# Performance work log

Measured on AMD Instinct MI355X. Metric: run time of the kernel, lower is better.

## Reference

```python
import jax, jax.numpy as jnp
import numpy as np

B, T, D = 16, 2048, 512
NUM_CODES = 8192
BETA = 0.25


def setup_inputs() -> dict:
    key = jax.random.key(0)
    k1, k2 = jax.random.split(key)
    z_e = jax.random.normal(k1, (B, T, D), dtype=jnp.float32)
    # nn.init.uniform_(weight, -1/num_codes, 1/num_codes)
    lim = 1.0 / NUM_CODES
    codebook = jax.random.uniform(k2, (NUM_CODES, D), dtype=jnp.float32,
                                  minval=-lim, maxval=lim)
    return {"z_e": z_e, "codebook": codebook}


def reference(z_e, codebook):
    b, t, d = z_e.shape
    flat = z_e.reshape(b * t, d)                      # [BT, D]
    dist = (jnp.sum(flat * flat, axis=1, keepdims=True)
            - 2.0 * (flat @ codebook.T)
            + jnp.sum(codebook * codebook, axis=1)[None, :])
    ids = jnp.argmin(dist, axis=1)                    # [BT]
    z_q = codebook[ids].reshape(b, t, d)              # gather + reshape
    codebook_loss = jnp.mean((z_q - jax.lax.stop_gradient(z_e)) ** 2)
    commit_loss = jnp.mean((z_e - jax.lax.stop_gradient(z_q)) ** 2)
    vq_loss = codebook_loss + BETA * commit_loss
    # straight-through estimator
    z_q_st = z_e + jax.lax.stop_gradient(z_q - z_e)
    return (z_q_st, ids.reshape(b, t), vq_loss)
```

## Files before the change

### kernel.cpp

```cpp
#include <hip/hip_runtime.h>

#define ROWS 32768
#define D 512
#define NCODES 8192
#define KC 384
#define NTILES 64
#define NSLOT 64

typedef _Float16 h8 __attribute__((ext_vector_type(8)));
typedef float f4v __attribute__((ext_vector_type(4)));

__global__ __launch_bounds__(256)
void k_prep(const float* __restrict__ zE, const float* __restrict__ cb,
            _Float16* __restrict__ zh, _Float16* __restrict__ ch,
            float* __restrict__ sq, float* __restrict__ e2,
            float* __restrict__ sabs, int* __restrict__ cnt,
            int* __restrict__ tileCnt) {
    const int wid  = blockIdx.x * 4 + (threadIdx.x >> 6);
    const int lane = threadIdx.x & 63;
    const bool isrow = wid < ROWS;
    const float* p = isrow ? zE + (size_t)wid * D
                           : cb + (size_t)(wid - ROWS) * D;

    {
        float4 u = *(const float4*)(p + lane * 8);
        float4 v = *(const float4*)(p + lane * 8 + 4);
        if (isrow) {
            h8 o = {(_Float16)u.x, (_Float16)u.y, (_Float16)u.z, (_Float16)u.w,
                    (_Float16)v.x, (_Float16)v.y, (_Float16)v.z, (_Float16)v.w};
            *(h8*)(zh + (size_t)wid * D + lane * 8) = o;
        } else {
            h8 o = {(_Float16)(u.x * 4096.0f), (_Float16)(u.y * 4096.0f),
                    (_Float16)(u.z * 4096.0f), (_Float16)(u.w * 4096.0f),
                    (_Float16)(v.x * 4096.0f), (_Float16)(v.y * 4096.0f),
                    (_Float16)(v.z * 4096.0f), (_Float16)(v.w * 4096.0f)};
            *(h8*)(ch + (size_t)(wid - ROWS) * D + lane * 8) = o;
        }
    }

    float v;
    if (lane < 32) {
        const int b = lane >> 3, j = lane & 7;
        const float* q = p + b * 128 + j;
        float r = __fmul_rn(q[0], q[0]);
#pragma unroll
        for (int i = 1; i < 16; ++i) {
            float t = q[i * 8];
            r = __fadd_rn(r, __fmul_rn(t, t));
        }
        v = r;
    } else {
        const int m = lane - 32;
        float sa = 0.0f;
#pragma unroll
        for (int i = 0; i < 16; ++i) sa += fabsf(p[i * 32 + m]);
        v = sa;
    }
    v = __fadd_rn(v, __shfl_xor(v, 1));
    v = __fadd_rn(v, __shfl_xor(v, 2));
    v = __fadd_rn(v, __shfl_xor(v, 4));
    v = __fadd_rn(v, __shfl_xor(v, 8));
    v = __fadd_rn(v, __shfl_xor(v, 16));
    float sa = __shfl(v, 32);
    if (lane == 0) {
        if (isrow) { sq[wid] = v; sabs[wid] = sa; cnt[wid] = 0; }
        else       { e2[wid - ROWS] = v; }
    }
    if (lane == 1 && wid < NTILES) tileCnt[wid] = 0;
}

__device__ __forceinline__ float dapprox(float s, float accv, float ecv) {
    float m = __fmul_rn(accv, 0.000244140625f);
    return __fadd_rn(__fsub_rn(s, __fmul_rn(2.0f, m)), ecv);
}

__global__ __launch_bounds__(256, 2)
void k_mfma_min(const _Float16* __restrict__ zh, const _Float16* __restrict__ ch,
                const float* __restrict__ sq, const float* __restrict__ e2,
                float* __restrict__ tmin) {
    __shared__ h8 AB[3 * 1536];

    const int p    = blockIdx.x;
    const int ct   = (p & 7) * 8 + ((p >> 3) & 7);
    const int rt   = p >> 6;
    const int wvu  = __builtin_amdgcn_readfirstlane(threadIdx.x >> 6);
    const int lane = threadIdx.x & 63;
    const int l15  = lane & 15;
    const int lk   = lane >> 4;
    const int rw   = rt * 256 + wvu * 64;
    const int cw   = ct * 128;

    f4v acc[4][8];
#pragma unroll
    for (int a = 0; a < 4; ++a)
#pragma unroll
        for (int b = 0; b < 8; ++b) acc[a][b] = (f4v){0.f, 0.f, 0.f, 0.f};

#define STAGE(buf, k0c)                                                              \
    {                                                                                \
        const int bb0 = (buf) * 1536;                                                \
        _Pragma("unroll")                                                            \
        for (int a = 0; a < 4; ++a) {                                                \
            const _Float16* src = zh + (size_t)(rw + a * 16 + l15) * D + (k0c) + lk * 8; \
            __builtin_amdgcn_global_load_lds(                                        \
                (const __attribute__((address_space(1))) void*)(const void*)src,    \
                (__attribute__((address_space(3))) void*)(void*)&AB[bb0 + wvu * 256 + a * 64], \
                16, 0, 0);                                                           \
        }                                                                            \
        _Pragma("unroll")                                                            \
        for (int j = 0; j < 2; ++j) {                                                \
            const int bb = wvu * 2 + j;                                              \
            const _Float16* src = ch + (size_t)(cw + bb * 16 + l15) * D + (k0c) + lk * 8; \
            __builtin_amdgcn_global_load_lds(                                        \
                (const __attribute__((address_space(1))) void*)(const void*)src,    \
                (__attribute__((address_space(3))) void*)(void*)&AB[bb0 + 1024 + bb * 64], \
                16, 0, 0);                                                           \
        }                                                                            \
    }

    STAGE(0, 0);
    STAGE(1, 32);

#pragma unroll 1
    for (int ks = 0; ks < 16; ++ks) {
        const int cur = ks % 3;
        __builtin_amdgcn_sched_barrier(0);
        if (ks < 15) {
            asm volatile("s_waitcnt vmcnt(6)" ::: "memory");
        } else {
            asm volatile("s_waitcnt vmcnt(0)" ::: "memory");
        }
        __builtin_amdgcn_sched_barrier(0);
        __builtin_amdgcn_s_barrier();
        __builtin_amdgcn_sched_barrier(0);
        if (ks < 14) STAGE((ks + 2) % 3, (ks + 2) * 32);

        h8 bf[8];
#pragma unroll
        for (int b = 0; b < 8; ++b) bf[b] = AB[cur * 1536 + 1024 + b * 64 + lane];
#pragma unroll
        for (int a = 0; a < 4; ++a) {
            h8 af = AB[cur * 1536 + wvu * 256 + a * 64 + lane];
#pragma unroll
            for (int b = 0; b < 8; ++b)
                acc[a][b] = __builtin_amdgcn_mfma_f32_16x16x32_f16(af, bf[b], acc[a][b], 0, 0, 0);
        }
    }
#undef STAGE

#pragma unroll
    for (int a = 0; a < 4; ++a) {
        const int r0 = rw + a * 16 + lk * 4;
        float s0 = sq[r0 + 0], s1 = sq[r0 + 1], s2 = sq[r0 + 2], s3 = sq[r0 + 3];
        float rm[4] = {INFINITY, INFINITY, INFINITY, INFINITY};
#pragma unroll
        for (int b = 0; b < 8; ++b) {
            float ecv = e2[cw + b * 16 + l15];
            rm[0] = fminf(rm[0], dapprox(s0, acc[a][b][0], ecv));
            rm[1] = fminf(rm[1], dapprox(s1, acc[a][b][1], ecv));
            rm[2] = fminf(rm[2], dapprox(s2, acc[a][b][2], ecv));
            rm[3] = fminf(rm[3], dapprox(s3, acc[a][b][3], ecv));
        }
#pragma unroll
        for (int jj = 0; jj < 4; ++jj) {
            float v = rm[jj];
            v = fminf(v, __shfl_xor(v, 1));
            v = fminf(v, __shfl_xor(v, 2));
            v = fminf(v, __shfl_xor(v, 4));
            v = fminf(v, __shfl_xor(v, 8));
            if (l15 == 0) tmin[(size_t)ct * ROWS + (r0 + jj)] = v;
        }
    }
}

__global__ __launch_bounds__(256)
void k_select(const float* __restrict__ tmin, const float* __restrict__ sabs,
              float* __restrict__ thr, int* __restrict__ tileCnt,
              int* __restrict__ tileRows) {
    __shared__ int           lcnt[NTILES];
    __shared__ int           lbase[NTILES];
    __shared__ unsigned char lrow[NTILES][256];

    const int tid     = threadIdx.x;
    const int rowBase = blockIdx.x * 256;
    const int row     = rowBase + tid;

    if (tid < NTILES) lcnt[tid] = 0;
    __syncthreads();

    float g = tmin[row];
#pragma unroll 8
    for (int i = 1; i < NTILES; ++i) g = fminf(g, tmin[(size_t)i * ROWS + row]);
    float th = g + (sabs[row] * 8e-7f + 6e-4f);
    thr[row] = th;
    for (int i = 0; i < NTILES; ++i)
        if (tmin[(size_t)i * ROWS + row] <= th) {
            int pos = atomicAdd(&lcnt[i], 1);
            lrow[i][pos] = (unsigned char)tid;
        }
    __syncthreads();

    if (tid < NTILES && lcnt[tid] > 0)
        lbase[tid] = atomicAdd(&tileCnt[tid], lcnt[tid]);
    __syncthreads();

    for (int i = 0; i < NTILES; ++i) {
        int n = lcnt[i];
        for (int j = tid; j < n; j += 256)
            tileRows[(size_t)i * ROWS + lbase[i] + j] = rowBase + lrow[i][j];
    }
}

__global__ __launch_bounds__(256, 2)
void k_mfma_cand(const _Float16* __restrict__ zh, const _Float16* __restrict__ ch,
                 const float* __restrict__ sq, const float* __restrict__ e2,
                 const float* __restrict__ thr, const int* __restrict__ tileCnt,
                 const int* __restrict__ tileRows, int* __restrict__ cnt,
                 int* __restrict__ cands) {
    const int p     = blockIdx.x;
    const int t     = (p & 7) * 8 + ((p >> 3) & 7);
    const int chunk = p >> 6;
    const int wave  = threadIdx.x >> 6;
    const int lane  = threadIdx.x & 63;
    const int l15   = lane & 15;
    const int lk    = lane >> 4;
    const int cw    = t * 128;
    const int n     = tileCnt[t];
    const int ngrp  = (n + 63) >> 6;

    for (int g = chunk * 4 + wave; g < ngrp; g += 32) {
        int gi = g * 64 + lane;
        int myrow = (gi < n) ? tileRows[(size_t)t * ROWS + gi] : -1;

        f4v acc[4][8];
#pragma unroll
        for (int a = 0; a < 4; ++a)
#pragma unroll
            for (int b = 0; b < 8; ++b) acc[a][b] = (f4v){0.f, 0.f, 0.f, 0.f};

#pragma unroll 2
        for (int k0 = 0; k0 < D; k0 += 32) {
            h8 bf[8];
#pragma unroll
            for (int b = 0; b < 8; ++b)
                bf[b] = *(const h8*)(ch + (size_t)(cw + b * 16 + l15) * D + k0 + lk * 8);
#pragma unroll
            for (int a = 0; a < 4; ++a) {
                int ra = __shfl(myrow, a * 16 + l15);
                ra = ra < 0 ? 0 : ra;
                h8 af = *(const h8*)(zh + (size_t)ra * D + k0 + lk * 8);
#pragma unroll
                for (int b = 0; b < 8; ++b)
                    acc[a][b] = __builtin_amdgcn_mfma_f32_16x16x32_f16(af, bf[b], acc[a][b], 0, 0, 0);
            }
        }

#pragma unroll
        for (int a = 0; a < 4; ++a) {
#pragma unroll
            for (int jj = 0; jj < 4; ++jj) {
                int rowv = __shfl(myrow, a * 16 + lk * 4 + jj);
                if (rowv < 0) continue;
                float s  = sq[rowv];
                float th = thr[rowv];
#pragma unroll
                for (int b = 0; b < 8; ++b) {
                    int c = cw + b * 16 + l15;
                    float d = dapprox(s, acc[a][b][jj], e2[c]);
                    if (d <= th) {
                        int sl = atomicAdd(&cnt[rowv], 1);
                        if (sl < NSLOT) cands[(size_t)rowv * NSLOT + sl] = c;
                    }
                }
            }
        }
    }
}

__device__ __forceinline__ float exact_d(const float* __restrict__ xr,
                                         const float* __restrict__ er,
                                         float s, float ev) {
    float m1 = 0.0f, m2 = 0.0f;
#pragma unroll 8
    for (int k = 0; k < KC; ++k) m1 = __builtin_fmaf(xr[k], er[k], m1);
#pragma unroll 8
    for (int k = KC; k < D; ++k) m2 = __builtin_fmaf(xr[k], er[k], m2);
    float m = __fadd_rn(m1, m2);
    return __fadd_rn(__fsub_rn(s, __fmul_rn(2.0f, m)), ev);
}

__global__ __launch_bounds__(256)
void k_rescore(const float* __restrict__ zE, const float* __restrict__ cb,
               const float* __restrict__ sq, const float* __restrict__ e2,
               const int* __restrict__ cnt, const int* __restrict__ cands,
               int* __restrict__ ids, float* __restrict__ outIds) {
    __shared__ float xs[4][D];
    const int wave = threadIdx.x >> 6;
    const int lane = threadIdx.x & 63;
    const int row  = blockIdx.x * 4 + wave;

    const float* xr = zE + (size_t)row * D;
    *(float4*)&xs[wave][lane * 8]     = *(const float4*)(xr + lane * 8);
    *(float4*)&xs[wave][lane * 8 + 4] = *(const float4*)(xr + lane * 8 + 4);
    __syncthreads();

    float s = sq[row];
    int   n = cnt[row];
    float bd = INFINITY;
    int   bi = NCODES - 1;
    if (n <= NSLOT) {
        for (int t = lane; t < n; t += 64) {
            int c = cands[(size_t)row * NSLOT + t];
            float d = exact_d(xs[wave], cb + (size_t)c * D, s, e2[c]);
            if (d < bd || (d == bd && c < bi)) { bd = d; bi = c; }
        }
    } else {
        for (int c = lane; c < NCODES; c += 64) {
            float d = exact_d(xs[wave], cb + (size_t)c * D, s, e2[c]);
            if (d < bd || (d == bd && c < bi)) { bd = d; bi = c; }
        }
    }
#pragma unroll
    for (int off = 32; off; off >>= 1) {
        float v2 = __shfl_xor(bd, off);
        int   x2 = __shfl_xor(bi, off);
        if (v2 < bd || (v2 == bd && x2 < bi)) { bd = v2; bi = x2; }
    }
    if (lane == 0) {
        int b = bi < 0 ? 0 : (bi > NCODES - 1 ? NCODES - 1 : bi);
        ids[row] = b;
        outIds[row] = (float)b;
    }
}

__global__ void k_gather(const float* __restrict__ zE, const float* __restrict__ cb,
                         const int* __restrict__ ids, float* __restrict__ outZ,
                         double* __restrict__ lossPart) {
    const int tid = threadIdx.x;
    double acc = 0.0;
#pragma unroll
    for (int it = 0; it < 4; ++it) {
        int chunk = blockIdx.x * 256 + tid + it * 1048576;
        int row   = chunk >> 7;
        int koff  = (chunk & 127) << 2;
        int id    = ids[row];
        id = id < 0 ? 0 : (id > NCODES - 1 ? NCODES - 1 : id);
        float4 ze = *(const float4*)(zE + ((size_t)row << 9) + koff);
        float4 zq = *(const float4*)(cb + ((size_t)id << 9) + koff);
        float d0 = __fsub_rn(zq.x, ze.x);
        float d1 = __fsub_rn(zq.y, ze.y);
        float d2 = __fsub_rn(zq.z, ze.z);
        float d3 = __fsub_rn(zq.w, ze.w);
        float4 v;
        v.x = __fadd_rn(ze.x, d0);
        v.y = __fadd_rn(ze.y, d1);
        v.z = __fadd_rn(ze.z, d2);
        v.w = __fadd_rn(ze.w, d3);
        *reinterpret_cast<float4*>(outZ + ((size_t)chunk << 2)) = v;
        acc += (double)d0 * d0 + (double)d1 * d1 + (double)d2 * d2 + (double)d3 * d3;
    }
    for (int off = 32; off; off >>= 1) acc += __shfl_down(acc, off);
    __shared__ double sred[4];
    if ((tid & 63) == 0) sred[tid >> 6] = acc;
    __syncthreads();
    if (tid == 0) lossPart[blockIdx.x] = (sred[0] + sred[1]) + (sred[2] + sred[3]);
}

__global__ void k_loss(const double* __restrict__ lossPart, float* __restrict__ outLoss) {
    const int tid = threadIdx.x;
    double acc = 0.0;
    for (int i = tid; i < 4096; i += 256) acc += lossPart[i];
    for (int off = 32; off; off >>= 1) acc += __shfl_down(acc, off);
    __shared__ double sred[4];
    if ((tid & 63) == 0) sred[tid >> 6] = acc;
    __syncthreads();
    if (tid == 0) {
        double mean = ((sred[0] + sred[1]) + (sred[2] + sred[3])) / 16777216.0;
        float cl = (float)mean;
        *outLoss = __fadd_rn(cl, __fmul_rn(0.25f, cl));
    }
}

extern "C" void kernel_launch(void* const* d_in, const int* in_sizes, int n_in,
                              void* d_out, int out_size, void* d_ws, size_t ws_size,
                              hipStream_t stream) {
    (void)in_sizes; (void)n_in; (void)out_size; (void)ws_size;
    const float* zE = (const float*)d_in[0];
    const float* cb = (const float*)d_in[1];
    float* out = (float*)d_out;
    char*  ws  = (char*)d_ws;
    char*  ob  = (char*)d_out;

    float*  sq       = (float*)(ws + 0);
    float*  e2       = (float*)(ws + 131072);
    int*    ids      = (int*)(ws + 163840);
    float*  sabs     = (float*)(ws + 294912);
    int*    tileCnt  = (int*)(ws + 425984);
    float*  thr      = (float*)(ws + 430080);
    int*    cnt      = (int*)(ws + 561152);
    double* lossPart = (double*)(ws + 1343488);

    _Float16* zh       = (_Float16*)(ob + 0);
    _Float16* ch       = (_Float16*)(ob + 33554432);
    float*    tmin     = (float*)(ob + 41943040);
    int*      tileRows = (int*)(ob + 50331648);
    int*      cands    = (int*)(ob + 58720256);

    k_prep<<<(ROWS + NCODES) / 4, 256, 0, stream>>>(zE, cb, zh, ch, sq, e2, sabs,
                                                    cnt, tileCnt);
    k_mfma_min<<<8192, 256, 0, stream>>>(zh, ch, sq, e2, tmin);
    k_select<<<ROWS / 256, 256, 0, stream>>>(tmin, sabs, thr, tileCnt, tileRows);
    k_mfma_cand<<<512, 256, 0, stream>>>(zh, ch, sq, e2, thr, tileCnt, tileRows,
                                         cnt, cands);
    k_rescore<<<ROWS / 4, 256, 0, stream>>>(zE, cb, sq, e2, cnt, cands,
                                            ids, out + 16777216);
    k_gather<<<4096, 256, 0, stream>>>(zE, cb, ids, out, lossPart);
    k_loss<<<1, 256, 0, stream>>>(lossPart, out + 16777216 + 32768);
}
```

Baseline: 691.6 us.

## Load A operand directly into registers, keep only codebook tiles in LDS

Each wave reads only its own 64 rows of the A operand, so staging A through shared memory is redundant. A fragments now go straight from global memory into a pair of register buffers that alternate between iterations, and only the codebook B tiles stay triple-buffered in LDS. The wait count is lowered to match the new number of in-flight loads, and the k-loop is fully unrolled so the register ping-pong resolves at compile time. This cuts LDS footprint and LDS read/write traffic, at the cost of more vector registers and direct global-load latency on the MFMA critical path.

```diff
diff --git a/kernel.cpp b/kernel.cpp
--- a/kernel.cpp
+++ b/kernel.cpp
@@ -78,7 +78,7 @@
 void k_mfma_min(const _Float16* __restrict__ zh, const _Float16* __restrict__ ch,
                 const float* __restrict__ sq, const float* __restrict__ e2,
                 float* __restrict__ tmin) {
-    __shared__ h8 AB[3 * 1536];
+    __shared__ h8 Bs[3][512];
 
     const int p    = blockIdx.x;
     const int ct   = (p & 7) * 8 + ((p >> 3) & 7);
@@ -96,57 +96,66 @@
 #pragma unroll
         for (int b = 0; b < 8; ++b) acc[a][b] = (f4v){0.f, 0.f, 0.f, 0.f};
 
-#define STAGE(buf, k0c)                                                              \
+#define STAGE_B(buf, k0c)                                                            \
     {                                                                                \
-        const int bb0 = (buf) * 1536;                                                \
-        _Pragma("unroll")                                                            \
-        for (int a = 0; a < 4; ++a) {                                                \
-            const _Float16* src = zh + (size_t)(rw + a * 16 + l15) * D + (k0c) + lk * 8; \
-            __builtin_amdgcn_global_load_lds(                                        \
-                (const __attribute__((address_space(1))) void*)(const void*)src,    \
-                (__attribute__((address_space(3))) void*)(void*)&AB[bb0 + wvu * 256 + a * 64], \
-                16, 0, 0);                                                           \
-        }                                                                            \
         _Pragma("unroll")                                                            \
         for (int j = 0; j < 2; ++j) {                                                \
             const int bb = wvu * 2 + j;                                              \
             const _Float16* src = ch + (size_t)(cw + bb * 16 + l15) * D + (k0c) + lk * 8; \
             __builtin_amdgcn_global_load_lds(                                        \
                 (const __attribute__((address_space(1))) void*)(const void*)src,    \
-                (__attribute__((address_space(3))) void*)(void*)&AB[bb0 + 1024 + bb * 64], \
+                (__attribute__((address_space(3))) void*)(void*)&Bs[buf][bb * 64],  \
                 16, 0, 0);                                                           \
         }                                                                            \
     }
-
-    STAGE(0, 0);
-    STAGE(1, 32);
-
-#pragma unroll 1
+#define LOADA(dst, k0c)                                                              \
+    {                                                                                \
+        _Pragma("unroll")                                                            \
+        for (int a = 0; a < 4; ++a)                                                  \
+            dst[a] = *(const h8*)(zh + (size_t)(rw + a * 16 + l15) * D + (k0c) + lk * 8); \
+    }
+#define COMPUTE(AREG, curb)                                                          \
+    {                                                                                \
+        h8 bf[8];                                                                    \
+        _Pragma("unroll")                                                            \
+        for (int b = 0; b < 8; ++b) bf[b] = Bs[curb][b * 64 + lane];                 \
+        _Pragma("unroll")                                                            \
+        for (int a = 0; a < 4; ++a) {                                                \
+            _Pragma("unroll")                                                        \
+            for (int b = 0; b < 8; ++b)                                              \
+                acc[a][b] = __builtin_amdgcn_mfma_f32_16x16x32_f16(AREG[a], bf[b], acc[a][b], 0, 0, 0); \
+        }                                                                            \
+    }
+
+    h8 aA[4], aB[4];
+    STAGE_B(0, 0);
+    LOADA(aA, 0);
+    STAGE_B(1, 32);
+
+#pragma unroll
     for (int ks = 0; ks < 16; ++ks) {
         const int cur = ks % 3;
         __builtin_amdgcn_sched_barrier(0);
         if (ks < 15) {
-            asm volatile("s_waitcnt vmcnt(6)" ::: "memory");
+            asm volatile("s_waitcnt vmcnt(2)" ::: "memory");
         } else {
             asm volatile("s_waitcnt vmcnt(0)" ::: "memory");
         }
         __builtin_amdgcn_sched_barrier(0);
         __builtin_amdgcn_s_barrier();
         __builtin_amdgcn_sched_barrier(0);
-        if (ks < 14) STAGE((ks + 2) % 3, (ks + 2) * 32);
-
-        h8 bf[8];
-#pragma unroll
-        for (int b = 0; b < 8; ++b) bf[b] = AB[cur * 1536 + 1024 + b * 64 + lane];
-#pragma unroll
-        for (int a = 0; a < 4; ++a) {
-            h8 af = AB[cur * 1536 + wvu * 256 + a * 64 + lane];
-#pragma unroll
-            for (int b = 0; b < 8; ++b)
-                acc[a][b] = __builtin_amdgcn_mfma_f32_16x16x32_f16(af, bf[b], acc[a][b], 0, 0, 0);
-        }
-    }
-#undef STAGE
+        if (ks < 15) {
+            if (ks & 1) LOADA(aA, (ks + 1) * 32)
+            else        LOADA(aB, (ks + 1) * 32)
+        }
+        if (ks < 14) STAGE_B((ks + 2) % 3, (ks + 2) * 32);
+
+        if (ks & 1) COMPUTE(aB, cur)
+        else        COMPUTE(aA, cur)
+    }
+#undef STAGE_B
+#undef LOADA
+#undef COMPUTE
 
 #pragma unroll
     for (int a = 0; a < 4; ++a) {
```

Result: slower. 732.3 us (+5.9%).
